# Performance work log

Hardware: AMD Instinct MI355X
Metric: run time of the kernel (lower is better)

Reference implementation:

```python
import jax, jax.numpy as jnp
import numpy as np

ISO = 0.5
CORNER_OFF = np.array([[0,0,0],[1,0,0],[1,1,0],[0,1,0],[0,0,1],[1,0,1],[1,1,1],[0,1,1]], np.float32)
EDGE_C = np.array([[0,1],[1,2],[2,3],[3,0],[4,5],[5,6],[6,7],[7,4],[0,4],[1,5],[2,6],[3,7]], np.int32)
TRI = [[],[0,8,3],[0,1,9],[1,8,3,9,8,1],[1,2,10],[0,8,3,1,2,10],[9,2,10,0,2,9],[2,8,3,2,10,8,10,9,8],[3,11,2],[0,11,2,8,11,0],[1,9,0,2,3,11],[1,11,2,1,9,11,9,8,11],[3,10,1,11,10,3],[0,10,1,0,8,10,8,11,10],[3,9,0,3,11,9,11,10,9],[9,8,10,10,8,11],[4,7,8],[4,3,0,7,3,4],[0,1,9,8,4,7],[4,1,9,4,7,1,7,3,1],[1,2,10,8,4,7],[3,4,7,3,0,4,1,2,10],[9,2,10,9,0,2,8,4,7],[2,10,9,2,9,7,2,7,3,7,9,4],[8,4,7,3,11,2],[11,4,7,11,2,4,2,0,4],[9,0,1,8,4,7,2,3,11],[4,7,11,9,4,11,9,11,2,9,2,1],[3,10,1,3,11,10,7,8,4],[1,11,10,1,4,11,1,0,4,7,11,4],[4,7,8,9,0,11,9,11,10,11,0,3],[4,7,11,4,11,9,9,11,10],[9,5,4],[9,5,4,0,8,3],[0,5,4,1,5,0],[8,5,4,8,3,5,3,1,5],[1,2,10,9,5,4],[3,0,8,1,2,10,4,9,5],[5,2,10,5,4,2,4,0,2],[2,10,5,3,2,5,3,5,4,3,4,8],[9,5,4,2,3,11],[0,11,2,0,8,11,4,9,5],[0,5,4,0,1,5,2,3,11],[2,1,5,2,5,8,2,8,11,4,8,5],[10,3,11,10,1,3,9,5,4],[4,9,5,0,8,1,8,10,1,8,11,10],[5,4,0,5,0,11,5,11,10,11,0,3],[5,4,8,5,8,10,10,8,11],[9,7,8,5,7,9],[9,3,0,9,5,3,5,7,3],[0,7,8,0,1,7,1,5,7],[1,5,3,3,5,7],[9,7,8,9,5,7,10,1,2],[10,1,2,9,5,0,5,3,0,5,7,3],[8,0,2,8,2,5,8,5,7,10,5,2],[2,10,5,2,5,3,3,5,7],[7,9,5,7,8,9,3,11,2],[9,5,7,9,7,2,9,2,0,2,7,11],[2,3,11,0,1,8,1,7,8,1,5,7],[11,2,1,11,1,7,7,1,5],[9,5,8,8,5,7,10,1,3,10,3,11],[5,7,0,5,0,9,7,11,0,1,0,10,11,10,0],[11,10,0,11,0,3,10,5,0,8,0,7,5,7,0],[11,10,5,7,11,5],[10,6,5],[0,8,3,5,10,6],[9,0,1,5,10,6],[1,8,3,1,9,8,5,10,6],[1,6,5,2,6,1],[1,6,5,1,2,6,3,0,8],[9,6,5,9,0,6,0,2,6],[5,9,8,5,8,2,5,2,6,3,2,8],[2,3,11,10,6,5],[11,0,8,11,2,0,10,6,5],[0,1,9,2,3,11,5,10,6],[5,10,6,1,9,2,9,11,2,9,8,11],[6,3,11,6,5,3,5,1,3],[0,8,11,0,11,5,0,5,1,5,11,6],[3,11,6,0,3,6,0,6,5,0,5,9],[6,5,9,6,9,11,11,9,8],[5,10,6,4,7,8],[4,3,0,4,7,3,6,5,10],[1,9,0,5,10,6,8,4,7],[10,6,5,1,9,7,1,7,3,7,9,4],[6,1,2,6,5,1,4,7,8],[1,2,5,5,2,6,3,0,4,3,4,7],[8,4,7,9,0,5,0,6,5,0,2,6],[7,3,9,7,9,4,3,2,9,5,9,6,2,6,9],[3,11,2,7,8,4,10,6,5],[5,10,6,4,7,2,4,2,0,2,7,11],[0,1,9,4,7,8,2,3,11,5,10,6],[9,2,1,9,11,2,9,4,11,7,11,4,5,10,6],[8,4,7,3,11,5,3,5,1,5,11,6],[5,1,11,5,11,6,1,0,11,7,11,4,0,4,11],[0,5,9,0,6,5,0,3,6,11,6,3,8,4,7],[6,5,9,6,9,11,4,7,9,7,11,9],[10,4,9,6,4,10],[4,10,6,4,9,10,0,8,3],[10,0,1,10,6,0,6,4,0],[8,3,1,8,1,6,8,6,4,6,1,10],[1,4,9,1,2,4,2,6,4],[3,0,8,1,2,9,2,4,9,2,6,4],[0,2,4,4,2,6],[8,3,2,8,2,4,4,2,6],[10,4,9,10,6,4,11,2,3],[0,8,2,2,8,11,4,9,10,4,10,6],[3,11,2,0,1,6,0,6,4,6,1,10],[6,4,1,6,1,10,4,8,1,2,1,11,8,11,1],[9,6,4,9,3,6,9,1,3,11,6,3],[8,11,1,8,1,0,11,6,1,9,1,4,6,4,1],[3,11,6,3,6,0,0,6,4],[6,4,8,11,6,8],[7,10,6,7,8,10,8,9,10],[0,7,3,0,10,7,0,9,10,6,7,10],[10,6,7,1,10,7,1,7,8,1,8,0],[10,6,7,10,7,1,1,7,3],[1,2,6,1,6,8,1,8,9,8,6,7],[2,6,9,2,9,1,6,7,9,0,9,3,7,3,9],[7,8,0,7,0,6,6,0,2],[7,3,2,6,7,2],[2,3,11,10,6,8,10,8,9,8,6,7],[2,0,7,2,7,11,0,9,7,6,7,10,9,10,7],[1,8,0,1,7,8,1,10,7,6,7,10,2,3,11],[11,2,1,11,1,7,10,6,1,6,7,1],[8,9,6,8,6,7,9,1,6,11,6,3,1,3,6],[0,9,1,11,6,7],[7,8,0,7,0,6,3,11,0,11,6,0],[7,11,6],[7,6,11],[3,0,8,11,7,6],[0,1,9,11,7,6],[8,1,9,8,3,1,11,7,6],[10,1,2,6,11,7],[1,2,10,3,0,8,6,11,7],[2,9,0,2,10,9,6,11,7],[6,11,7,2,10,3,10,8,3,10,9,8],[7,2,3,6,2,7],[7,0,8,7,6,0,6,2,0],[2,7,6,2,3,7,0,1,9],[1,6,2,1,8,6,1,9,8,8,7,6],[10,7,6,10,1,7,1,3,7],[10,7,6,1,7,10,1,8,7,1,0,8],[0,3,7,0,7,10,0,10,9,6,10,7],[7,6,10,7,10,8,8,10,9],[6,8,4,11,8,6],[3,6,11,3,0,6,0,4,6],[8,6,11,8,4,6,9,0,1],[9,4,6,9,6,3,9,3,1,11,3,6],[6,8,4,6,11,8,2,10,1],[1,2,10,3,0,11,0,6,11,0,4,6],[4,11,8,4,6,11,0,2,9,2,10,9],[10,9,3,10,3,2,9,4,3,11,3,6,4,6,3],[8,2,3,8,4,2,4,6,2],[0,4,2,4,6,2],[1,9,0,2,3,4,2,4,6,4,3,8],[1,9,4,1,4,2,2,4,6],[8,1,3,8,6,1,8,4,6,6,10,1],[10,1,0,10,0,6,6,0,4],[4,6,3,4,3,8,6,10,3,0,3,9,10,9,3],[10,9,4,6,10,4],[4,9,5,7,6,11],[0,8,3,4,9,5,11,7,6],[5,0,1,5,4,0,7,6,11],[11,7,6,8,3,4,3,5,4,3,1,5],[9,5,4,10,1,2,7,6,11],[6,11,7,1,2,10,0,8,3,4,9,5],[7,6,11,5,4,10,4,2,10,4,0,2],[3,4,8,3,5,4,3,2,5,10,5,2,11,7,6],[7,2,3,7,6,2,5,4,9],[9,5,4,0,8,6,0,6,2,6,8,7],[3,6,2,3,7,6,1,5,0,5,4,0],[6,2,8,6,8,7,2,1,8,4,8,5,1,5,8],[9,5,4,10,1,6,1,7,6,1,3,7],[1,6,10,1,7,6,1,0,7,8,7,0,9,5,4],[4,0,10,4,10,5,0,3,10,6,10,7,3,7,10],[7,6,10,7,10,8,5,4,10,4,8,10],[6,9,5,6,11,9,11,8,9],[3,6,11,0,6,3,0,5,6,0,9,5],[0,11,8,0,5,11,0,1,5,5,6,11],[6,11,3,6,3,5,5,3,1],[1,2,10,9,5,11,9,11,8,11,5,6],[0,11,3,0,6,11,0,9,6,5,6,9,1,2,10],[11,8,5,11,5,6,8,0,5,10,5,2,0,2,5],[6,11,3,6,3,5,2,10,3,10,5,3],[5,8,9,5,2,8,5,6,2,3,8,2],[9,5,6,9,6,0,0,6,2],[1,5,8,1,8,0,5,6,8,3,8,2,6,2,8],[1,5,6,2,1,6],[1,3,6,1,6,10,3,8,6,5,6,9,8,9,6],[10,1,0,10,0,6,9,5,0,5,6,0],[0,3,8,5,6,10],[10,5,6],[11,5,10,7,5,11],[11,5,10,11,7,5,8,3,0],[5,11,7,5,10,11,1,9,0],[10,7,5,10,11,7,9,8,1,8,3,1],[11,1,2,11,7,1,7,5,1],[0,8,3,1,2,7,1,7,5,7,2,11],[9,7,5,9,2,7,9,0,2,2,11,7],[7,5,2,7,2,11,5,9,2,3,2,8,9,8,2],[2,5,10,2,3,5,3,7,5],[8,2,0,8,5,2,8,7,5,10,2,5],[9,0,1,5,10,3,5,3,7,3,10,2],[9,8,2,9,2,1,8,7,2,10,2,5,7,5,2],[1,3,5,3,7,5],[0,8,7,0,7,1,1,7,5],[9,0,3,9,3,5,5,3,7],[9,8,7,5,9,7],[5,8,4,5,10,8,10,11,8],[5,0,4,5,11,0,5,10,11,11,3,0],[0,1,9,8,4,10,8,10,11,10,4,5],[10,11,4,10,4,5,11,3,4,9,4,1,3,1,4],[2,5,1,2,8,5,2,11,8,4,5,8],[0,4,11,0,11,3,4,5,11,2,11,1,5,1,11],[0,2,5,0,5,9,2,11,5,4,5,8,11,8,5],[9,4,5,2,11,3],[2,5,10,3,5,2,3,4,5,3,8,4],[5,10,2,5,2,4,4,2,0],[3,10,2,3,5,10,3,8,5,4,5,8,0,1,9],[5,10,2,5,2,4,1,9,2,9,4,2],[8,4,5,8,5,3,3,5,1],[0,4,5,1,0,5],[8,4,5,8,5,3,9,0,5,0,3,5],[9,4,5],[4,11,7,4,9,11,9,10,11],[0,8,3,4,9,7,9,11,7,9,10,11],[1,10,11,1,11,4,1,4,0,7,4,11],[3,1,4,3,4,8,1,10,4,7,4,11,10,11,4],[4,11,7,9,11,4,9,2,11,9,1,2],[9,7,4,9,11,7,9,1,11,2,11,1,0,8,3],[11,7,4,11,4,2,2,4,0],[11,7,4,11,4,2,8,3,4,3,2,4],[2,9,10,2,7,9,2,3,7,7,4,9],[9,10,7,9,7,4,10,2,7,8,7,0,2,0,7],[3,7,10,3,10,2,7,4,10,1,10,0,4,0,10],[1,10,2,8,7,4],[4,9,1,4,1,7,7,1,3],[4,9,1,4,1,7,0,8,1,8,7,1],[4,0,3,7,4,3],[4,8,7],[9,10,8,10,11,8],[3,0,9,3,9,11,11,9,10],[0,1,10,0,10,8,8,10,11],[3,1,10,11,3,10],[1,2,11,1,11,9,9,11,8],[3,0,9,3,9,11,1,2,9,2,11,9],[0,2,11,8,0,11],[3,2,11],[2,3,8,2,8,10,10,8,9],[9,10,2,0,9,2],[2,3,8,2,8,10,0,1,8,1,10,8],[1,10,2],[1,3,8,9,1,8],[0,9,1],[0,3,8],[]]
TRI_TABLE = np.full((256, 16), -1, np.int32)
for _i, _r in enumerate(TRI):
    TRI_TABLE[_i, :len(_r)] = _r


def setup_inputs() -> dict:
    key = jax.random.key(0)
    volume = jax.random.uniform(key, (128, 128, 128), dtype=jnp.float32)
    return {"volume": volume}


def _marching_cubes(volume):
    D, H, W = volume.shape
    d, h, w = D - 1, H - 1, W - 1
    off_i = CORNER_OFF.astype(np.int32)
    cvals = jnp.stack([volume[o[2]:o[2]+d, o[1]:o[1]+h, o[0]:o[0]+w] for o in off_i], axis=-1).reshape(-1, 8)
    cube_idx = jnp.sum((cvals < ISO).astype(jnp.int32) * (1 << np.arange(8, dtype=np.int32)), axis=-1)
    zz, yy, xx = jnp.meshgrid(jnp.arange(d), jnp.arange(h), jnp.arange(w), indexing='ij')
    base = jnp.stack([xx, yy, zz], axis=-1).reshape(-1, 3).astype(jnp.float32)
    v1 = cvals[:, EDGE_C[:, 0]]
    v2 = cvals[:, EDGE_C[:, 1]]
    denom = v2 - v1
    safe = jnp.abs(denom) > 1e-9
    t = jnp.where(safe, (ISO - v1) / jnp.where(safe, denom, 1.0), 0.5)
    p1 = CORNER_OFF[EDGE_C[:, 0]]
    p2 = CORNER_OFF[EDGE_C[:, 1]]
    evert = base[:, None, :] + p1[None] + t[..., None] * (p2 - p1)[None]
    tri_edges = jnp.asarray(TRI_TABLE)[cube_idx][:, :15].reshape(-1, 5, 3)
    valid = tri_edges[:, :, 0] >= 0
    idx = jnp.maximum(tri_edges, 0)
    N = evert.shape[0]
    verts = evert[jnp.arange(N)[:, None, None], idx]
    verts = verts * valid[..., None, None].astype(verts.dtype)
    vertices = verts.reshape(-1, 3)
    tri_valid = valid.reshape(-1)
    num_triangles = jnp.sum(tri_valid.astype(jnp.int32))
    return vertices, tri_valid, num_triangles


def reference(volume):
    return _marching_cubes(volume)
```

## Files before the change

kernel.cpp:

```cpp
#include <hip/hip_runtime.h>

#define DIMV 128
#define CDIM 127
static constexpr long long NCELL = 127LL * 127LL * 127LL;
static constexpr long long VTX_FLOATS = NCELL * 45;
static constexpr long long CNT_OFF = NCELL * 50;
static constexpr int NBLK = (int)((NCELL + 255) / 256);
static constexpr int FULL_BLOCKS = (int)(NCELL / 256);

#define P1  -1
#define P4  -1,-1,-1,-1
#define P7  -1,-1,-1,-1,-1,-1,-1
#define P10 -1,-1,-1,-1,-1,-1,-1,-1,-1,-1
#define P13 -1,-1,-1,-1,-1,-1,-1,-1,-1,-1,-1,-1,-1
#define P16 -1,-1,-1,-1,-1,-1,-1,-1,-1,-1,-1,-1,-1,-1,-1,-1

__device__ __align__(16) const signed char TRI_TBL[256][16] = {
{P16},
{0,8,3,P13},
{0,1,9,P13},
{1,8,3,9,8,1,P10},
{1,2,10,P13},
{0,8,3,1,2,10,P10},
{9,2,10,0,2,9,P10},
{2,8,3,2,10,8,10,9,8,P7},
{3,11,2,P13},
{0,11,2,8,11,0,P10},
{1,9,0,2,3,11,P10},
{1,11,2,1,9,11,9,8,11,P7},
{3,10,1,11,10,3,P10},
{0,10,1,0,8,10,8,11,10,P7},
{3,9,0,3,11,9,11,10,9,P7},
{9,8,10,10,8,11,P10},
{4,7,8,P13},
{4,3,0,7,3,4,P10},
{0,1,9,8,4,7,P10},
{4,1,9,4,7,1,7,3,1,P7},
{1,2,10,8,4,7,P10},
{3,4,7,3,0,4,1,2,10,P7},
{9,2,10,9,0,2,8,4,7,P7},
{2,10,9,2,9,7,2,7,3,7,9,4,P4},
{8,4,7,3,11,2,P10},
{11,4,7,11,2,4,2,0,4,P7},
{9,0,1,8,4,7,2,3,11,P7},
{4,7,11,9,4,11,9,11,2,9,2,1,P4},
{3,10,1,3,11,10,7,8,4,P7},
{1,11,10,1,4,11,1,0,4,7,11,4,P4},
{4,7,8,9,0,11,9,11,10,11,0,3,P4},
{4,7,11,4,11,9,9,11,10,P7},
{9,5,4,P13},
{9,5,4,0,8,3,P10},
{0,5,4,1,5,0,P10},
{8,5,4,8,3,5,3,1,5,P7},
{1,2,10,9,5,4,P10},
{3,0,8,1,2,10,4,9,5,P7},
{5,2,10,5,4,2,4,0,2,P7},
{2,10,5,3,2,5,3,5,4,3,4,8,P4},
{9,5,4,2,3,11,P10},
{0,11,2,0,8,11,4,9,5,P7},
{0,5,4,0,1,5,2,3,11,P7},
{2,1,5,2,5,8,2,8,11,4,8,5,P4},
{10,3,11,10,1,3,9,5,4,P7},
{4,9,5,0,8,1,8,10,1,8,11,10,P4},
{5,4,0,5,0,11,5,11,10,11,0,3,P4},
{5,4,8,5,8,10,10,8,11,P7},
{9,7,8,5,7,9,P10},
{9,3,0,9,5,3,5,7,3,P7},
{0,7,8,0,1,7,1,5,7,P7},
{1,5,3,3,5,7,P10},
{9,7,8,9,5,7,10,1,2,P7},
{10,1,2,9,5,0,5,3,0,5,7,3,P4},
{8,0,2,8,2,5,8,5,7,10,5,2,P4},
{2,10,5,2,5,3,3,5,7,P7},
{7,9,5,7,8,9,3,11,2,P7},
{9,5,7,9,7,2,9,2,0,2,7,11,P4},
{2,3,11,0,1,8,1,7,8,1,5,7,P4},
{11,2,1,11,1,7,7,1,5,P7},
{9,5,8,8,5,7,10,1,3,10,3,11,P4},
{5,7,0,5,0,9,7,11,0,1,0,10,11,10,0,P1},
{11,10,0,11,0,3,10,5,0,8,0,7,5,7,0,P1},
{11,10,5,7,11,5,P10},
{10,6,5,P13},
{0,8,3,5,10,6,P10},
{9,0,1,5,10,6,P10},
{1,8,3,1,9,8,5,10,6,P7},
{1,6,5,2,6,1,P10},
{1,6,5,1,2,6,3,0,8,P7},
{9,6,5,9,0,6,0,2,6,P7},
{5,9,8,5,8,2,5,2,6,3,2,8,P4},
{2,3,11,10,6,5,P10},
{11,0,8,11,2,0,10,6,5,P7},
{0,1,9,2,3,11,5,10,6,P7},
{5,10,6,1,9,2,9,11,2,9,8,11,P4},
{6,3,11,6,5,3,5,1,3,P7},
{0,8,11,0,11,5,0,5,1,5,11,6,P4},
{3,11,6,0,3,6,0,6,5,0,5,9,P4},
{6,5,9,6,9,11,11,9,8,P7},
{5,10,6,4,7,8,P10},
{4,3,0,4,7,3,6,5,10,P7},
{1,9,0,5,10,6,8,4,7,P7},
{10,6,5,1,9,7,1,7,3,7,9,4,P4},
{6,1,2,6,5,1,4,7,8,P7},
{1,2,5,5,2,6,3,0,4,3,4,7,P4},
{8,4,7,9,0,5,0,6,5,0,2,6,P4},
{7,3,9,7,9,4,3,2,9,5,9,6,2,6,9,P1},
{3,11,2,7,8,4,10,6,5,P7},
{5,10,6,4,7,2,4,2,0,2,7,11,P4},
{0,1,9,4,7,8,2,3,11,5,10,6,P4},
{9,2,1,9,11,2,9,4,11,7,11,4,5,10,6,P1},
{8,4,7,3,11,5,3,5,1,5,11,6,P4},
{5,1,11,5,11,6,1,0,11,7,11,4,0,4,11,P1},
{0,5,9,0,6,5,0,3,6,11,6,3,8,4,7,P1},
{6,5,9,6,9,11,4,7,9,7,11,9,P4},
{10,4,9,6,4,10,P10},
{4,10,6,4,9,10,0,8,3,P7},
{10,0,1,10,6,0,6,4,0,P7},
{8,3,1,8,1,6,8,6,4,6,1,10,P4},
{1,4,9,1,2,4,2,6,4,P7},
{3,0,8,1,2,9,2,4,9,2,6,4,P4},
{0,2,4,4,2,6,P10},
{8,3,2,8,2,4,4,2,6,P7},
{10,4,9,10,6,4,11,2,3,P7},
{0,8,2,2,8,11,4,9,10,4,10,6,P4},
{3,11,2,0,1,6,0,6,4,6,1,10,P4},
{6,4,1,6,1,10,4,8,1,2,1,11,8,11,1,P1},
{9,6,4,9,3,6,9,1,3,11,6,3,P4},
{8,11,1,8,1,0,11,6,1,9,1,4,6,4,1,P1},
{3,11,6,3,6,0,0,6,4,P7},
{6,4,8,11,6,8,P10},
{7,10,6,7,8,10,8,9,10,P7},
{0,7,3,0,10,7,0,9,10,6,7,10,P4},
{10,6,7,1,10,7,1,7,8,1,8,0,P4},
{10,6,7,10,7,1,1,7,3,P7},
{1,2,6,1,6,8,1,8,9,8,6,7,P4},
{2,6,9,2,9,1,6,7,9,0,9,3,7,3,9,P1},
{7,8,0,7,0,6,6,0,2,P7},
{7,3,2,6,7,2,P10},
{2,3,11,10,6,8,10,8,9,8,6,7,P4},
{2,0,7,2,7,11,0,9,7,6,7,10,9,10,7,P1},
{1,8,0,1,7,8,1,10,7,6,7,10,2,3,11,P1},
{11,2,1,11,1,7,10,6,1,6,7,1,P4},
{8,9,6,8,6,7,9,1,6,11,6,3,1,3,6,P1},
{0,9,1,11,6,7,P10},
{7,8,0,7,0,6,3,11,0,11,6,0,P4},
{7,11,6,P13},
{7,6,11,P13},
{3,0,8,11,7,6,P10},
{0,1,9,11,7,6,P10},
{8,1,9,8,3,1,11,7,6,P7},
{10,1,2,6,11,7,P10},
{1,2,10,3,0,8,6,11,7,P7},
{2,9,0,2,10,9,6,11,7,P7},
{6,11,7,2,10,3,10,8,3,10,9,8,P4},
{7,2,3,6,2,7,P10},
{7,0,8,7,6,0,6,2,0,P7},
{2,7,6,2,3,7,0,1,9,P7},
{1,6,2,1,8,6,1,9,8,8,7,6,P4},
{10,7,6,10,1,7,1,3,7,P7},
{10,7,6,1,7,10,1,8,7,1,0,8,P4},
{0,3,7,0,7,10,0,10,9,6,10,7,P4},
{7,6,10,7,10,8,8,10,9,P7},
{6,8,4,11,8,6,P10},
{3,6,11,3,0,6,0,4,6,P7},
{8,6,11,8,4,6,9,0,1,P7},
{9,4,6,9,6,3,9,3,1,11,3,6,P4},
{6,8,4,6,11,8,2,10,1,P7},
{1,2,10,3,0,11,0,6,11,0,4,6,P4},
{4,11,8,4,6,11,0,2,9,2,10,9,P4},
{10,9,3,10,3,2,9,4,3,11,3,6,4,6,3,P1},
{8,2,3,8,4,2,4,6,2,P7},
{0,4,2,4,6,2,P10},
{1,9,0,2,3,4,2,4,6,4,3,8,P4},
{1,9,4,1,4,2,2,4,6,P7},
{8,1,3,8,6,1,8,4,6,6,10,1,P4},
{10,1,0,10,0,6,6,0,4,P7},
{4,6,3,4,3,8,6,10,3,0,3,9,10,9,3,P1},
{10,9,4,6,10,4,P10},
{4,9,5,7,6,11,P10},
{0,8,3,4,9,5,11,7,6,P7},
{5,0,1,5,4,0,7,6,11,P7},
{11,7,6,8,3,4,3,5,4,3,1,5,P4},
{9,5,4,10,1,2,7,6,11,P7},
{6,11,7,1,2,10,0,8,3,4,9,5,P4},
{7,6,11,5,4,10,4,2,10,4,0,2,P4},
{3,4,8,3,5,4,3,2,5,10,5,2,11,7,6,P1},
{7,2,3,7,6,2,5,4,9,P7},
{9,5,4,0,8,6,0,6,2,6,8,7,P4},
{3,6,2,3,7,6,1,5,0,5,4,0,P4},
{6,2,8,6,8,7,2,1,8,4,8,5,1,5,8,P1},
{9,5,4,10,1,6,1,7,6,1,3,7,P4},
{1,6,10,1,7,6,1,0,7,8,7,0,9,5,4,P1},
{4,0,10,4,10,5,0,3,10,6,10,7,3,7,10,P1},
{7,6,10,7,10,8,5,4,10,4,8,10,P4},
{6,9,5,6,11,9,11,8,9,P7},
{3,6,11,0,6,3,0,5,6,0,9,5,P4},
{0,11,8,0,5,11,0,1,5,5,6,11,P4},
{6,11,3,6,3,5,5,3,1,P7},
{1,2,10,9,5,11,9,11,8,11,5,6,P4},
{0,11,3,0,6,11,0,9,6,5,6,9,1,2,10,P1},
{11,8,5,11,5,6,8,0,5,10,5,2,0,2,5,P1},
{6,11,3,6,3,5,2,10,3,10,5,3,P4},
{5,8,9,5,2,8,5,6,2,3,8,2,P4},
{9,5,6,9,6,0,0,6,2,P7},
{1,5,8,1,8,0,5,6,8,3,8,2,6,2,8,P1},
{1,5,6,2,1,6,P10},
{1,3,6,1,6,10,3,8,6,5,6,9,8,9,6,P1},
{10,1,0,10,0,6,9,5,0,5,6,0,P4},
{0,3,8,5,6,10,P10},
{10,5,6,P13},
{11,5,10,7,5,11,P10},
{11,5,10,11,7,5,8,3,0,P7},
{5,11,7,5,10,11,1,9,0,P7},
{10,7,5,10,11,7,9,8,1,8,3,1,P4},
{11,1,2,11,7,1,7,5,1,P7},
{0,8,3,1,2,7,1,7,5,7,2,11,P4},
{9,7,5,9,2,7,9,0,2,2,11,7,P4},
{7,5,2,7,2,11,5,9,2,3,2,8,9,8,2,P1},
{2,5,10,2,3,5,3,7,5,P7},
{8,2,0,8,5,2,8,7,5,10,2,5,P4},
{9,0,1,5,10,3,5,3,7,3,10,2,P4},
{9,8,2,9,2,1,8,7,2,10,2,5,7,5,2,P1},
{1,3,5,3,7,5,P10},
{0,8,7,0,7,1,1,7,5,P7},
{9,0,3,9,3,5,5,3,7,P7},
{9,8,7,5,9,7,P10},
{5,8,4,5,10,8,10,11,8,P7},
{5,0,4,5,11,0,5,10,11,11,3,0,P4},
{0,1,9,8,4,10,8,10,11,10,4,5,P4},
{10,11,4,10,4,5,11,3,4,9,4,1,3,1,4,P1},
{2,5,1,2,8,5,2,11,8,4,5,8,P4},
{0,4,11,0,11,3,4,5,11,2,11,1,5,1,11,P1},
{0,2,5,0,5,9,2,11,5,4,5,8,11,8,5,P1},
{9,4,5,2,11,3,P10},
{2,5,10,3,5,2,3,4,5,3,8,4,P4},
{5,10,2,5,2,4,4,2,0,P7},
{3,10,2,3,5,10,3,8,5,4,5,8,0,1,9,P1},
{5,10,2,5,2,4,1,9,2,9,4,2,P4},
{8,4,5,8,5,3,3,5,1,P7},
{0,4,5,1,0,5,P10},
{8,4,5,8,5,3,9,0,5,0,3,5,P4},
{9,4,5,P13},
{4,11,7,4,9,11,9,10,11,P7},
{0,8,3,4,9,7,9,11,7,9,10,11,P4},
{1,10,11,1,11,4,1,4,0,7,4,11,P4},
{3,1,4,3,4,8,1,10,4,7,4,11,10,11,4,P1},
{4,11,7,9,11,4,9,2,11,9,1,2,P4},
{9,7,4,9,11,7,9,1,11,2,11,1,0,8,3,P1},
{11,7,4,11,4,2,2,4,0,P7},
{11,7,4,11,4,2,8,3,4,3,2,4,P4},
{2,9,10,2,7,9,2,3,7,7,4,9,P4},
{9,10,7,9,7,4,10,2,7,8,7,0,2,0,7,P1},
{3,7,10,3,10,2,7,4,10,1,10,0,4,0,10,P1},
{1,10,2,8,7,4,P10},
{4,9,1,4,1,7,7,1,3,P7},
{4,9,1,4,1,7,0,8,1,8,7,1,P4},
{4,0,3,7,4,3,P10},
{4,8,7,P13},
{9,10,8,10,11,8,P10},
{3,0,9,3,9,11,11,9,10,P7},
{0,1,10,0,10,8,8,10,11,P7},
{3,1,10,11,3,10,P10},
{1,2,11,1,11,9,9,11,8,P7},
{3,0,9,3,9,11,1,2,9,2,11,9,P4},
{0,2,11,8,0,11,P10},
{3,2,11,P13},
{2,3,8,2,8,10,10,8,9,P7},
{9,10,2,0,9,2,P10},
{2,3,8,2,8,10,0,1,8,1,10,8,P4},
{1,10,2,P13},
{1,3,8,9,1,8,P10},
{0,9,1,P13},
{0,3,8,P13},
{P16}
};

#define MAX_ 0x666
#define MBX_ 0x633
#define MAY_ 0xCCC
#define MBY_ 0xC66
#define MAZ_ 0x0F0
#define MBZ_ 0xFF0

__global__ __launch_bounds__(256) void mc_kernel(const float* __restrict__ vol,
                                                 float* __restrict__ out,
                                                 int* __restrict__ ws) {
    __shared__ __align__(16) float exp_s[256 * 45];
    __shared__ unsigned char tvm_s[256];

    const int tid  = threadIdx.x;
    const int w    = tid >> 6;
    const int lane = tid & 63;
    const long long cell = (long long)blockIdx.x * 256 + tid;
    const bool active = cell < NCELL;

    const int x = (int)(cell % CDIM);
    const int r = (int)(cell / CDIM);
    const int y = r % CDIM;
    const int z = r / CDIM;
    const float xf = (float)x, yf = (float)y, zf = (float)z;

    int4 row = make_int4(-1, -1, -1, -1);
    float tv[12];
#pragma unroll
    for (int e = 0; e < 12; ++e) tv[e] = 0.0f;

    if (active) {
        const float* p = vol + ((size_t)z * DIMV + y) * DIMV + x;
        float cv[8];
        cv[0] = p[0];
        cv[1] = p[1];
        cv[3] = p[DIMV];
        cv[2] = p[DIMV + 1];
        cv[4] = p[DIMV * DIMV];
        cv[5] = p[DIMV * DIMV + 1];
        cv[7] = p[DIMV * DIMV + DIMV];
        cv[6] = p[DIMV * DIMV + DIMV + 1];

        int cidx = 0;
#pragma unroll
        for (int k = 0; k < 8; ++k)
            cidx |= (cv[k] < 0.5f) ? (1 << k) : 0;

        row = ((const int4*)TRI_TBL)[cidx];

        const int EA[12] = {0,1,2,3,4,5,6,7,0,1,2,3};
        const int EB[12] = {1,2,3,0,5,6,7,4,4,5,6,7};
#pragma unroll
        for (int e = 0; e < 12; ++e) {
            const float v1 = cv[EA[e]];
            const float v2 = cv[EB[e]];
            const float d  = v2 - v1;
            tv[e] = (fabsf(d) > 1e-9f) ? ((0.5f - v1) / d) : 0.5f;
        }
    }

    const int rw[4] = {row.x, row.y, row.z, row.w};

    int m = 0;
#pragma unroll
    for (int t5 = 0; t5 < 5; ++t5) {
        const int b = 3 * t5;
        const int eb = (int)(signed char)((rw[b >> 2] >> ((b & 3) * 8)) & 0xFF);
        m |= (eb >= 0) ? (1 << t5) : 0;
    }
    tvm_s[tid] = (unsigned char)m;
    int cnt = __popc(m);

    float* ep = &exp_s[tid * 45];
#pragma unroll
    for (int b = 0; b < 15; ++b) {
        const int eb = (int)(signed char)((rw[b >> 2] >> ((b & 3) * 8)) & 0xFF);
        const bool ok = (eb >= 0);
        const int ec = ok ? eb : 12;

        const bool s0 = (ec & 1) != 0;
        const bool s1 = (ec & 2) != 0;
        const bool s2 = (ec & 4) != 0;
        const bool s3 = (ec & 8) != 0;
        const float p0 = s0 ? tv[1]  : tv[0];
        const float p1 = s0 ? tv[3]  : tv[2];
        const float p2 = s0 ? tv[5]  : tv[4];
        const float p3 = s0 ? tv[7]  : tv[6];
        const float p4 = s0 ? tv[9]  : tv[8];
        const float p5 = s0 ? tv[11] : tv[10];
        const float q0 = s1 ? p1 : p0;
        const float q1 = s1 ? p3 : p2;
        const float q2 = s1 ? p5 : p4;
        const float h0 = s2 ? q1 : q0;
        const float t  = s3 ? q2 : h0;

        const int ax = (MAX_ >> ec) & 1, bx = (MBX_ >> ec) & 1;
        const int ay = (MAY_ >> ec) & 1, by = (MBY_ >> ec) & 1;
        const int az = (MAZ_ >> ec) & 1, bz = (MBZ_ >> ec) & 1;
        float vx = (xf + (float)ax) + t * (float)(bx - ax);
        float vy = (yf + (float)ay) + t * (float)(by - ay);
        float vz = (zf + (float)az) + t * (float)(bz - az);
        ep[3*b + 0] = ok ? vx : 0.0f;
        ep[3*b + 1] = ok ? vy : 0.0f;
        ep[3*b + 2] = ok ? vz : 0.0f;
    }

#pragma unroll
    for (int off = 32; off > 0; off >>= 1)
        cnt += __shfl_down(cnt, off);
    if (lane == 0)
        ws[blockIdx.x * 4 + w] = cnt;

    asm volatile("s_waitcnt lgkmcnt(0)" ::: "memory");
    __builtin_amdgcn_sched_barrier(0);

    const size_t base45 = (size_t)blockIdx.x * (256 * 45);
    float4* vout = (float4*)(out + base45);
    const float4* vin = (const float4*)exp_s;

    if (blockIdx.x < FULL_BLOCKS) {
        const int wb4 = w * 720;
#pragma unroll
        for (int k = 0; k < 11; ++k)
            vout[wb4 + k * 64 + lane] = vin[wb4 + k * 64 + lane];
        if (lane < 16)
            vout[wb4 + 704 + lane] = vin[wb4 + 704 + lane];

        float* tvout = out + VTX_FLOATS + (size_t)blockIdx.x * (256 * 5);
#pragma unroll
        for (int k = 0; k < 5; ++k) {
            const int i = w * 320 + k * 64 + lane;
            const uint c  = (uint)i / 5u;
            const uint t5 = (uint)i - c * 5u;
            tvout[i] = ((tvm_s[c] >> t5) & 1) ? 1.0f : 0.0f;
        }
    } else {
        __syncthreads();
        const int nfull4 = 1428;
        for (int i4 = tid; i4 < nfull4; i4 += 256)
            vout[i4] = vin[i4];
        if (tid < 3)
            out[base45 + 5712 + tid] = exp_s[5712 + tid];

        float* tvout = out + VTX_FLOATS + (size_t)blockIdx.x * (256 * 5);
        const int ntv = 127 * 5;
#pragma unroll
        for (int k = 0; k < 3; ++k) {
            const int i = tid + k * 256;
            if (i < ntv) {
                const uint c  = (uint)i / 5u;
                const uint t5 = (uint)i - c * 5u;
                tvout[i] = ((tvm_s[c] >> t5) & 1) ? 1.0f : 0.0f;
            }
        }
    }
}

__global__ __launch_bounds__(1024) void sum_kernel(const int* __restrict__ ws,
                                                   float* __restrict__ out) {
    __shared__ int sh[16];
    const int tid = threadIdx.x;
    int s = 0;
    for (int i = tid; i < NBLK * 4; i += 1024)
        s += ws[i];
#pragma unroll
    for (int off = 32; off > 0; off >>= 1)
        s += __shfl_down(s, off);
    if ((tid & 63) == 0) sh[tid >> 6] = s;
    __syncthreads();
    if (tid == 0) {
        int tot = 0;
#pragma unroll
        for (int k = 0; k < 16; ++k) tot += sh[k];
        out[CNT_OFF] = (float)tot;
    }
}

extern "C" void kernel_launch(void* const* d_in, const int* in_sizes, int n_in,
                              void* d_out, int out_size, void* d_ws, size_t ws_size,
                              hipStream_t stream) {
    const float* vol = (const float*)d_in[0];
    float* out = (float*)d_out;
    int* ws = (int*)d_ws;

    mc_kernel<<<NBLK, 256, 0, stream>>>(vol, out, ws);
    sum_kernel<<<1, 1024, 0, stream>>>(ws, out);
}
```

Measured before the change: 88.56 us.

## Stage vertex output per wave in two halves to halve shared memory

Each wave now expands only 32 cells at a time into its own 32x45-float shared buffer and copies that to global memory, then does the same for the other 32 lanes. This halves the block's LDS footprint, so more blocks can be resident per CU and more stores are in flight. The tail block drops its __syncthreads and uses per-wave bounded scalar copies instead. The cost is an extra wait-and-store phase per wave, and the two halves of the cell expansion now run one after the other.

Result: slower. 107.4 us (+21.2%).

```diff
diff --git a/kernel.cpp b/kernel.cpp
--- a/kernel.cpp
+++ b/kernel.cpp
@@ -281,72 +281,9 @@
 #define MAZ_ 0x0F0
 #define MBZ_ 0xFF0
 
-__global__ __launch_bounds__(256) void mc_kernel(const float* __restrict__ vol,
-                                                 float* __restrict__ out,
-                                                 int* __restrict__ ws) {
-    __shared__ __align__(16) float exp_s[256 * 45];
-    __shared__ unsigned char tvm_s[256];
-
-    const int tid  = threadIdx.x;
-    const int w    = tid >> 6;
-    const int lane = tid & 63;
-    const long long cell = (long long)blockIdx.x * 256 + tid;
-    const bool active = cell < NCELL;
-
-    const int x = (int)(cell % CDIM);
-    const int r = (int)(cell / CDIM);
-    const int y = r % CDIM;
-    const int z = r / CDIM;
-    const float xf = (float)x, yf = (float)y, zf = (float)z;
-
-    int4 row = make_int4(-1, -1, -1, -1);
-    float tv[12];
-#pragma unroll
-    for (int e = 0; e < 12; ++e) tv[e] = 0.0f;
-
-    if (active) {
-        const float* p = vol + ((size_t)z * DIMV + y) * DIMV + x;
-        float cv[8];
-        cv[0] = p[0];
-        cv[1] = p[1];
-        cv[3] = p[DIMV];
-        cv[2] = p[DIMV + 1];
-        cv[4] = p[DIMV * DIMV];
-        cv[5] = p[DIMV * DIMV + 1];
-        cv[7] = p[DIMV * DIMV + DIMV];
-        cv[6] = p[DIMV * DIMV + DIMV + 1];
-
-        int cidx = 0;
-#pragma unroll
-        for (int k = 0; k < 8; ++k)
-            cidx |= (cv[k] < 0.5f) ? (1 << k) : 0;
-
-        row = ((const int4*)TRI_TBL)[cidx];
-
-        const int EA[12] = {0,1,2,3,4,5,6,7,0,1,2,3};
-        const int EB[12] = {1,2,3,0,5,6,7,4,4,5,6,7};
-#pragma unroll
-        for (int e = 0; e < 12; ++e) {
-            const float v1 = cv[EA[e]];
-            const float v2 = cv[EB[e]];
-            const float d  = v2 - v1;
-            tv[e] = (fabsf(d) > 1e-9f) ? ((0.5f - v1) / d) : 0.5f;
-        }
-    }
-
-    const int rw[4] = {row.x, row.y, row.z, row.w};
-
-    int m = 0;
-#pragma unroll
-    for (int t5 = 0; t5 < 5; ++t5) {
-        const int b = 3 * t5;
-        const int eb = (int)(signed char)((rw[b >> 2] >> ((b & 3) * 8)) & 0xFF);
-        m |= (eb >= 0) ? (1 << t5) : 0;
-    }
-    tvm_s[tid] = (unsigned char)m;
-    int cnt = __popc(m);
-
-    float* ep = &exp_s[tid * 45];
+__device__ __forceinline__ void expand_cell(float* ep, const int rw[4],
+                                            const float tv[12],
+                                            float xf, float yf, float zf) {
 #pragma unroll
     for (int b = 0; b < 15; ++b) {
         const int eb = (int)(signed char)((rw[b >> 2] >> ((b & 3) * 8)) & 0xFF);
@@ -379,6 +316,72 @@
         ep[3*b + 1] = ok ? vy : 0.0f;
         ep[3*b + 2] = ok ? vz : 0.0f;
     }
+}
+
+__global__ __launch_bounds__(256) void mc_kernel(const float* __restrict__ vol,
+                                                 float* __restrict__ out,
+                                                 int* __restrict__ ws) {
+    __shared__ __align__(16) float buf_s[4][32 * 45];
+    __shared__ unsigned char tvm_s[256];
+
+    const int tid  = threadIdx.x;
+    const int w    = tid >> 6;
+    const int lane = tid & 63;
+    const long long cell = (long long)blockIdx.x * 256 + tid;
+    const bool active = cell < NCELL;
+
+    const int x = (int)(cell % CDIM);
+    const int r = (int)(cell / CDIM);
+    const int y = r % CDIM;
+    const int z = r / CDIM;
+    const float xf = (float)x, yf = (float)y, zf = (float)z;
+
+    int4 row = make_int4(-1, -1, -1, -1);
+    float tv[12];
+#pragma unroll
+    for (int e = 0; e < 12; ++e) tv[e] = 0.0f;
+
+    if (active) {
+        const float* p = vol + ((size_t)z * DIMV + y) * DIMV + x;
+        float cv[8];
+        cv[0] = p[0];
+        cv[1] = p[1];
+        cv[3] = p[DIMV];
+        cv[2] = p[DIMV + 1];
+        cv[4] = p[DIMV * DIMV];
+        cv[5] = p[DIMV * DIMV + 1];
+        cv[7] = p[DIMV * DIMV + DIMV];
+        cv[6] = p[DIMV * DIMV + DIMV + 1];
+
+        int cidx = 0;
+#pragma unroll
+        for (int k = 0; k < 8; ++k)
+            cidx |= (cv[k] < 0.5f) ? (1 << k) : 0;
+
+        row = ((const int4*)TRI_TBL)[cidx];
+
+        const int EA[12] = {0,1,2,3,4,5,6,7,0,1,2,3};
+        const int EB[12] = {1,2,3,0,5,6,7,4,4,5,6,7};
+#pragma unroll
+        for (int e = 0; e < 12; ++e) {
+            const float v1 = cv[EA[e]];
+            const float v2 = cv[EB[e]];
+            const float d  = v2 - v1;
+            tv[e] = (fabsf(d) > 1e-9f) ? ((0.5f - v1) / d) : 0.5f;
+        }
+    }
+
+    const int rw[4] = {row.x, row.y, row.z, row.w};
+
+    int m = 0;
+#pragma unroll
+    for (int t5 = 0; t5 < 5; ++t5) {
+        const int b = 3 * t5;
+        const int eb = (int)(signed char)((rw[b >> 2] >> ((b & 3) * 8)) & 0xFF);
+        m |= (eb >= 0) ? (1 << t5) : 0;
+    }
+    tvm_s[tid] = (unsigned char)m;
+    int cnt = __popc(m);
 
 #pragma unroll
     for (int off = 32; off > 0; off >>= 1)
@@ -386,22 +389,57 @@
     if (lane == 0)
         ws[blockIdx.x * 4 + w] = cnt;
 
+    float* ep = &buf_s[w][(lane & 31) * 45];
+    const float4* vinw = (const float4*)&buf_s[w][0];
+    const size_t base45 = (size_t)blockIdx.x * (256 * 45);
+    float4* voutw = (float4*)(out + base45 + (size_t)w * 2880);
+
+    const bool full = (blockIdx.x < FULL_BLOCKS);
+
+    if (lane < 32)
+        expand_cell(ep, rw, tv, xf, yf, zf);
     asm volatile("s_waitcnt lgkmcnt(0)" ::: "memory");
     __builtin_amdgcn_sched_barrier(0);
 
-    const size_t base45 = (size_t)blockIdx.x * (256 * 45);
-    float4* vout = (float4*)(out + base45);
-    const float4* vin = (const float4*)exp_s;
-
-    if (blockIdx.x < FULL_BLOCKS) {
-        const int wb4 = w * 720;
-#pragma unroll
-        for (int k = 0; k < 11; ++k)
-            vout[wb4 + k * 64 + lane] = vin[wb4 + k * 64 + lane];
-        if (lane < 16)
-            vout[wb4 + 704 + lane] = vin[wb4 + 704 + lane];
-
-        float* tvout = out + VTX_FLOATS + (size_t)blockIdx.x * (256 * 5);
+    if (full) {
+#pragma unroll
+        for (int k = 0; k < 5; ++k)
+            voutw[k * 64 + lane] = vinw[k * 64 + lane];
+        if (lane < 40)
+            voutw[320 + lane] = vinw[320 + lane];
+    } else {
+        const int limit = (int)(NCELL - (long long)blockIdx.x * 256) * 45;
+        for (int fi = lane; fi < 1440; fi += 64) {
+            const int gf = w * 2880 + fi;
+            if (gf < limit)
+                out[base45 + gf] = buf_s[w][fi];
+        }
+    }
+
+    __builtin_amdgcn_sched_barrier(0);
+
+    if (lane >= 32)
+        expand_cell(ep, rw, tv, xf, yf, zf);
+    asm volatile("s_waitcnt lgkmcnt(0)" ::: "memory");
+    __builtin_amdgcn_sched_barrier(0);
+
+    if (full) {
+#pragma unroll
+        for (int k = 0; k < 5; ++k)
+            voutw[360 + k * 64 + lane] = vinw[k * 64 + lane];
+        if (lane < 40)
+            voutw[360 + 320 + lane] = vinw[320 + lane];
+    } else {
+        const int limit = (int)(NCELL - (long long)blockIdx.x * 256) * 45;
+        for (int fi = lane; fi < 1440; fi += 64) {
+            const int gf = w * 2880 + 1440 + fi;
+            if (gf < limit)
+                out[base45 + gf] = buf_s[w][fi];
+        }
+    }
+
+    float* tvout = out + VTX_FLOATS + (size_t)blockIdx.x * (256 * 5);
+    if (full) {
 #pragma unroll
         for (int k = 0; k < 5; ++k) {
             const int i = w * 320 + k * 64 + lane;
@@ -410,18 +448,10 @@
             tvout[i] = ((tvm_s[c] >> t5) & 1) ? 1.0f : 0.0f;
         }
     } else {
-        __syncthreads();
-        const int nfull4 = 1428;
-        for (int i4 = tid; i4 < nfull4; i4 += 256)
-            vout[i4] = vin[i4];
-        if (tid < 3)
-            out[base45 + 5712 + tid] = exp_s[5712 + tid];
-
-        float* tvout = out + VTX_FLOATS + (size_t)blockIdx.x * (256 * 5);
-        const int ntv = 127 * 5;
-#pragma unroll
-        for (int k = 0; k < 3; ++k) {
-            const int i = tid + k * 256;
+        const int ntv = (int)(NCELL - (long long)blockIdx.x * 256) * 5;
+#pragma unroll
+        for (int k = 0; k < 5; ++k) {
+            const int i = w * 320 + k * 64 + lane;
             if (i < ntv) {
                 const uint c  = (uint)i / 5u;
                 const uint t5 = (uint)i - c * 5u;
```

## Use persistent grid with 128-cell tiles, two threads per cell, double-buffered LDS

Applied to the files above, without the earlier changes.

Switches from one 256-thread block per 256 cells to a fixed grid of 768 persistent blocks that loop over 128-cell tiles. Two threads share each cell and split the 15 triangle-vertex slots, and the LDS staging buffer is double-buffered so one barrier per tile is enough. The aim is to cut launch and tail overhead, halve per-thread serial vertex work, and let each block's stores overlap the next tile's compute. In exchange, each thread now repeats the corner loads and edge interpolation, and every tile pays a workgroup barrier.

Result: slower. 116.5 us (+31.5%).

```diff
diff --git a/kernel.cpp b/kernel.cpp
--- a/kernel.cpp
+++ b/kernel.cpp
@@ -5,8 +5,8 @@
 static constexpr long long NCELL = 127LL * 127LL * 127LL;
 static constexpr long long VTX_FLOATS = NCELL * 45;
 static constexpr long long CNT_OFF = NCELL * 50;
-static constexpr int NBLK = (int)((NCELL + 255) / 256);
-static constexpr int FULL_BLOCKS = (int)(NCELL / 256);
+static constexpr int NTILES = (int)((NCELL + 127) / 128);
+static constexpr int GRID = 768;
 
 #define P1  -1
 #define P4  -1,-1,-1,-1
@@ -284,100 +284,157 @@
 __global__ __launch_bounds__(256) void mc_kernel(const float* __restrict__ vol,
                                                  float* __restrict__ out,
                                                  int* __restrict__ ws) {
-    __shared__ __align__(16) float exp_s[256 * 45];
-    __shared__ unsigned char tvm_s[256];
+    __shared__ __align__(16) float buf_s[2][128 * 45];
+    __shared__ unsigned char tvm_s[2][128];
 
     const int tid  = threadIdx.x;
     const int w    = tid >> 6;
     const int lane = tid & 63;
-    const long long cell = (long long)blockIdx.x * 256 + tid;
-    const bool active = cell < NCELL;
-
-    const int x = (int)(cell % CDIM);
-    const int r = (int)(cell / CDIM);
-    const int y = r % CDIM;
-    const int z = r / CDIM;
-    const float xf = (float)x, yf = (float)y, zf = (float)z;
-
-    int4 row = make_int4(-1, -1, -1, -1);
-    float tv[12];
-#pragma unroll
-    for (int e = 0; e < 12; ++e) tv[e] = 0.0f;
-
-    if (active) {
-        const float* p = vol + ((size_t)z * DIMV + y) * DIMV + x;
-        float cv[8];
-        cv[0] = p[0];
-        cv[1] = p[1];
-        cv[3] = p[DIMV];
-        cv[2] = p[DIMV + 1];
-        cv[4] = p[DIMV * DIMV];
-        cv[5] = p[DIMV * DIMV + 1];
-        cv[7] = p[DIMV * DIMV + DIMV];
-        cv[6] = p[DIMV * DIMV + DIMV + 1];
-
-        int cidx = 0;
-#pragma unroll
-        for (int k = 0; k < 8; ++k)
-            cidx |= (cv[k] < 0.5f) ? (1 << k) : 0;
-
-        row = ((const int4*)TRI_TBL)[cidx];
-
-        const int EA[12] = {0,1,2,3,4,5,6,7,0,1,2,3};
-        const int EB[12] = {1,2,3,0,5,6,7,4,4,5,6,7};
-#pragma unroll
-        for (int e = 0; e < 12; ++e) {
-            const float v1 = cv[EA[e]];
-            const float v2 = cv[EB[e]];
-            const float d  = v2 - v1;
-            tv[e] = (fabsf(d) > 1e-9f) ? ((0.5f - v1) / d) : 0.5f;
+    const int cl   = tid & 127;
+    const int p    = tid >> 7;
+    int cnt = 0;
+    int it = 0;
+
+    for (int tile = blockIdx.x; tile < NTILES; tile += GRID, ++it) {
+        const int cur = it & 1;
+
+        const long long cell = (long long)tile * 128 + cl;
+        const bool active = cell < NCELL;
+
+        const uint cc = (uint)(active ? cell : 0);
+        const uint x = cc % CDIM;
+        const uint r = cc / CDIM;
+        const uint y = r % CDIM;
+        const uint z = r / CDIM;
+        const float xf = (float)x, yf = (float)y, zf = (float)z;
+
+        int4 row = make_int4(-1, -1, -1, -1);
+        float tv[12];
+#pragma unroll
+        for (int e = 0; e < 12; ++e) tv[e] = 0.0f;
+
+        if (active) {
+            const float* pv = vol + ((size_t)z * DIMV + y) * DIMV + x;
+            float cv[8];
+            cv[0] = pv[0];
+            cv[1] = pv[1];
+            cv[3] = pv[DIMV];
+            cv[2] = pv[DIMV + 1];
+            cv[4] = pv[DIMV * DIMV];
+            cv[5] = pv[DIMV * DIMV + 1];
+            cv[7] = pv[DIMV * DIMV + DIMV];
+            cv[6] = pv[DIMV * DIMV + DIMV + 1];
+
+            int cidx = 0;
+#pragma unroll
+            for (int k = 0; k < 8; ++k)
+                cidx |= (cv[k] < 0.5f) ? (1 << k) : 0;
+
+            row = ((const int4*)TRI_TBL)[cidx];
+
+            const int EA[12] = {0,1,2,3,4,5,6,7,0,1,2,3};
+            const int EB[12] = {1,2,3,0,5,6,7,4,4,5,6,7};
+#pragma unroll
+            for (int e = 0; e < 12; ++e) {
+                const float v1 = cv[EA[e]];
+                const float v2 = cv[EB[e]];
+                const float d  = v2 - v1;
+                tv[e] = (fabsf(d) > 1e-9f) ? ((0.5f - v1) / d) : 0.5f;
+            }
         }
-    }
-
-    const int rw[4] = {row.x, row.y, row.z, row.w};
-
-    int m = 0;
-#pragma unroll
-    for (int t5 = 0; t5 < 5; ++t5) {
-        const int b = 3 * t5;
-        const int eb = (int)(signed char)((rw[b >> 2] >> ((b & 3) * 8)) & 0xFF);
-        m |= (eb >= 0) ? (1 << t5) : 0;
-    }
-    tvm_s[tid] = (unsigned char)m;
-    int cnt = __popc(m);
-
-    float* ep = &exp_s[tid * 45];
-#pragma unroll
-    for (int b = 0; b < 15; ++b) {
-        const int eb = (int)(signed char)((rw[b >> 2] >> ((b & 3) * 8)) & 0xFF);
-        const bool ok = (eb >= 0);
-        const int ec = ok ? eb : 12;
-
-        const bool s0 = (ec & 1) != 0;
-        const bool s1 = (ec & 2) != 0;
-        const bool s2 = (ec & 4) != 0;
-        const bool s3 = (ec & 8) != 0;
-        const float p0 = s0 ? tv[1]  : tv[0];
-        const float p1 = s0 ? tv[3]  : tv[2];
-        const float p2 = s0 ? tv[5]  : tv[4];
-        const float p3 = s0 ? tv[7]  : tv[6];
-        const float p4 = s0 ? tv[9]  : tv[8];
-        const float p5 = s0 ? tv[11] : tv[10];
-        const float q0 = s1 ? p1 : p0;
-        const float q1 = s1 ? p3 : p2;
-        const float q2 = s1 ? p5 : p4;
-        const float h0 = s2 ? q1 : q0;
-        const float t  = s3 ? q2 : h0;
-
-        const int ax = (MAX_ >> ec) & 1, bx = (MBX_ >> ec) & 1;
-        const int ay = (MAY_ >> ec) & 1, by = (MBY_ >> ec) & 1;
-        const int az = (MAZ_ >> ec) & 1, bz = (MBZ_ >> ec) & 1;
-        float vx = (xf + (float)ax) + t * (float)(bx - ax);
-        float vy = (yf + (float)ay) + t * (float)(by - ay);
-        float vz = (zf + (float)az) + t * (float)(bz - az);
-        ep[3*b + 0] = ok ? vx : 0.0f;
-        ep[3*b + 1] = ok ? vy : 0.0f;
-        ep[3*b + 2] = ok ? vz : 0.0f;
+
+        const int rw[4] = {row.x, row.y, row.z, row.w};
+
+        if (p == 0) {
+            int m = 0;
+#pragma unroll
+            for (int t5 = 0; t5 < 5; ++t5) {
+                const int b = 3 * t5;
+                const int eb = (int)(signed char)((rw[b >> 2] >> ((b & 3) * 8)) & 0xFF);
+                m |= (eb >= 0) ? (1 << t5) : 0;
+            }
+            tvm_s[cur][cl] = (unsigned char)m;
+            cnt += __popc(m);
+        }
+
+        float* ep = &buf_s[cur][cl * 45];
+#pragma unroll
+        for (int s = 0; s < 8; ++s) {
+            const int b = 2 * s + p;
+            if (b < 15) {
+                const int eb = (int)(signed char)((rw[b >> 2] >> ((b & 3) * 8)) & 0xFF);
+                const bool ok = (eb >= 0);
+                const int ec = ok ? eb : 12;
+
+                const bool s0 = (ec & 1) != 0;
+                const bool s1 = (ec & 2) != 0;
+                const bool s2 = (ec & 4) != 0;
+                const bool s3 = (ec & 8) != 0;
+                const float p0 = s0 ? tv[1]  : tv[0];
+                const float p1 = s0 ? tv[3]  : tv[2];
+                const float p2 = s0 ? tv[5]  : tv[4];
+                const float p3 = s0 ? tv[7]  : tv[6];
+                const float p4 = s0 ? tv[9]  : tv[8];
+                const float p5 = s0 ? tv[11] : tv[10];
+                const float q0 = s1 ? p1 : p0;
+                const float q1 = s1 ? p3 : p2;
+                const float q2 = s1 ? p5 : p4;
+                const float h0 = s2 ? q1 : q0;
+                const float t  = s3 ? q2 : h0;
+
+                const int ax = (MAX_ >> ec) & 1, bx = (MBX_ >> ec) & 1;
+                const int ay = (MAY_ >> ec) & 1, by = (MBY_ >> ec) & 1;
+                const int az = (MAZ_ >> ec) & 1, bz = (MBZ_ >> ec) & 1;
+                float vx = (xf + (float)ax) + t * (float)(bx - ax);
+                float vy = (yf + (float)ay) + t * (float)(by - ay);
+                float vz = (zf + (float)az) + t * (float)(bz - az);
+                ep[3*b + 0] = ok ? vx : 0.0f;
+                ep[3*b + 1] = ok ? vy : 0.0f;
+                ep[3*b + 2] = ok ? vz : 0.0f;
+            }
+        }
+
+        asm volatile("s_waitcnt lgkmcnt(0)" ::: "memory");
+        __builtin_amdgcn_s_barrier();
+        __builtin_amdgcn_sched_barrier(0);
+
+        const float4* vin = (const float4*)&buf_s[cur][0];
+        float4* vout = (float4*)out + (size_t)tile * 1440;
+
+        if (tile != NTILES - 1) {
+#pragma unroll
+            for (int k = 0; k < 5; ++k)
+                vout[k * 256 + tid] = vin[k * 256 + tid];
+            if (tid < 160)
+                vout[1280 + tid] = vin[1280 + tid];
+
+            float* tvout = out + VTX_FLOATS + (size_t)tile * 640;
+#pragma unroll
+            for (int k = 0; k < 3; ++k) {
+                const int i = k * 256 + tid;
+                if (k < 2 || tid < 128) {
+                    const uint c  = (uint)i / 5u;
+                    const uint t5 = (uint)i - c * 5u;
+                    tvout[i] = ((tvm_s[cur][c] >> t5) & 1) ? 1.0f : 0.0f;
+                }
+            }
+        } else {
+            const float* bs = &buf_s[cur][0];
+            const size_t vb = (size_t)tile * 5760;
+            for (int fi = tid; fi < 5715; fi += 256)
+                out[vb + fi] = bs[fi];
+            float* tvout = out + VTX_FLOATS + (size_t)tile * 640;
+#pragma unroll
+            for (int k = 0; k < 3; ++k) {
+                const int i = k * 256 + tid;
+                if (i < 635) {
+                    const uint c  = (uint)i / 5u;
+                    const uint t5 = (uint)i - c * 5u;
+                    tvout[i] = ((tvm_s[cur][c] >> t5) & 1) ? 1.0f : 0.0f;
+                }
+            }
+        }
+        __builtin_amdgcn_sched_barrier(0);
     }
 
 #pragma unroll
@@ -385,50 +442,6 @@
         cnt += __shfl_down(cnt, off);
     if (lane == 0)
         ws[blockIdx.x * 4 + w] = cnt;
-
-    asm volatile("s_waitcnt lgkmcnt(0)" ::: "memory");
-    __builtin_amdgcn_sched_barrier(0);
-
-    const size_t base45 = (size_t)blockIdx.x * (256 * 45);
-    float4* vout = (float4*)(out + base45);
-    const float4* vin = (const float4*)exp_s;
-
-    if (blockIdx.x < FULL_BLOCKS) {
-        const int wb4 = w * 720;
-#pragma unroll
-        for (int k = 0; k < 11; ++k)
-            vout[wb4 + k * 64 + lane] = vin[wb4 + k * 64 + lane];
-        if (lane < 16)
-            vout[wb4 + 704 + lane] = vin[wb4 + 704 + lane];
-
-        float* tvout = out + VTX_FLOATS + (size_t)blockIdx.x * (256 * 5);
-#pragma unroll
-        for (int k = 0; k < 5; ++k) {
-            const int i = w * 320 + k * 64 + lane;
-            const uint c  = (uint)i / 5u;
-            const uint t5 = (uint)i - c * 5u;
-            tvout[i] = ((tvm_s[c] >> t5) & 1) ? 1.0f : 0.0f;
-        }
-    } else {
-        __syncthreads();
-        const int nfull4 = 1428;
-        for (int i4 = tid; i4 < nfull4; i4 += 256)
-            vout[i4] = vin[i4];
-        if (tid < 3)
-            out[base45 + 5712 + tid] = exp_s[5712 + tid];
-
-        float* tvout = out + VTX_FLOATS + (size_t)blockIdx.x * (256 * 5);
-        const int ntv = 127 * 5;
-#pragma unroll
-        for (int k = 0; k < 3; ++k) {
-            const int i = tid + k * 256;
-            if (i < ntv) {
-                const uint c  = (uint)i / 5u;
-                const uint t5 = (uint)i - c * 5u;
-                tvout[i] = ((tvm_s[c] >> t5) & 1) ? 1.0f : 0.0f;
-            }
-        }
-    }
 }
 
 __global__ __launch_bounds__(1024) void sum_kernel(const int* __restrict__ ws,
@@ -436,7 +449,7 @@
     __shared__ int sh[16];
     const int tid = threadIdx.x;
     int s = 0;
-    for (int i = tid; i < NBLK * 4; i += 1024)
+    for (int i = tid; i < GRID * 4; i += 1024)
         s += ws[i];
 #pragma unroll
     for (int off = 32; off > 0; off >>= 1)
@@ -458,6 +471,6 @@
     float* out = (float*)d_out;
     int* ws = (int*)d_ws;
 
-    mc_kernel<<<NBLK, 256, 0, stream>>>(vol, out, ws);
+    mc_kernel<<<GRID, 256, 0, stream>>>(vol, out, ws);
     sum_kernel<<<1, 1024, 0, stream>>>(ws, out);
 }
```
